# Kernel tuning notes

Hardware: AMD Instinct MI355X
Metric: run time of the kernel (lower is better)

The kernel has to match this reference:

```python
import jax, jax.numpy as jnp
import numpy as np

DMODEL = 1024
NHEAD = 16
HDIM = DMODEL // NHEAD
CTXLEN = 2048
BATCH = 2


def setup_inputs() -> dict:
    key = jax.random.key(0)
    k_x, k_qkv, k_pw, k_pb = jax.random.split(key, 4)
    x = jax.random.normal(k_x, (BATCH, CTXLEN, DMODEL), dtype=jnp.float32)
    # nn.Linear weights: stored as [out, in]; init scale ~ 1/sqrt(in)
    s = 1.0 / np.sqrt(DMODEL)
    w_qkv = jax.random.uniform(k_qkv, (3 * DMODEL, DMODEL), minval=-s, maxval=s, dtype=jnp.float32)
    w_proj = jax.random.uniform(k_pw, (DMODEL, DMODEL), minval=-s, maxval=s, dtype=jnp.float32)
    b_proj = jax.random.uniform(k_pb, (DMODEL,), minval=-s, maxval=s, dtype=jnp.float32)
    return {"x": x, "w_qkv": w_qkv, "w_proj": w_proj, "b_proj": b_proj}


def reference(x, w_qkv, w_proj, b_proj):
    b, t, c = x.shape
    qkv = jnp.einsum('btc,oc->bto', x, w_qkv)  # [b, t, 3c]
    q, k, v = jnp.split(qkv, 3, axis=-1)
    # [b, nhead, t, hdim]
    q = q.reshape(b, t, NHEAD, HDIM).transpose(0, 2, 1, 3)
    k = k.reshape(b, t, NHEAD, HDIM).transpose(0, 2, 1, 3)
    v = v.reshape(b, t, NHEAD, HDIM).transpose(0, 2, 1, 3)
    # NOTE: original code MULTIPLIES by sqrt(hdim) (not the usual divide)
    att = jnp.einsum('bhqd,bhkd->bhqk', q, k) * (HDIM ** 0.5)
    causal = jnp.tril(jnp.ones((t, t), dtype=bool))  # [t, t]
    att = jnp.where(causal[None, None], att, -jnp.inf)
    att = jax.nn.softmax(att, axis=-1)
    y = jnp.einsum('bhqk,bhkd->bhqd', att, v)
    y = y.transpose(0, 2, 1, 3).reshape(b, t, c)
    return jnp.einsum('btc,oc->bto', y, w_proj) + b_proj
```

## Files before the change

### kernel.cpp

```cpp
#include <hip/hip_runtime.h>
#include <hip/hip_bf16.h>

#define DMODEL 1024
#define NHEAD 16
#define HDIM 64
#define CTXLEN 2048
#define BATCH 2
#define M_TOTAL (BATCH * CTXLEN)

typedef unsigned short ushort_t;
typedef __attribute__((ext_vector_type(8))) _Float16 f16x8;
typedef __attribute__((ext_vector_type(8))) unsigned short u16x8;
typedef __attribute__((ext_vector_type(4))) float f32x4;
typedef __attribute__((ext_vector_type(4))) unsigned short u16x4;

#define SCALE_LOG2 11.5415603271f

__device__ __forceinline__ unsigned short f32_f16(float f) {
    return __builtin_bit_cast(unsigned short, (_Float16)f);
}
__device__ __forceinline__ float f16_f32(unsigned short h) {
    return (float)__builtin_bit_cast(_Float16, h);
}
__device__ __forceinline__ float fast_exp2(float x) {
    return __builtin_amdgcn_exp2f(x);
}
__device__ __forceinline__ f32x4 mfma16f(f16x8 a, f16x8 b, f32x4 c) {
    return __builtin_amdgcn_mfma_f32_16x16x32_f16(a, b, c, 0, 0, 0);
}
__device__ __forceinline__ void gload_lds16(const ushort_t* g, ushort_t* l) {
    __builtin_amdgcn_global_load_lds(
        (const __attribute__((address_space(1))) void*)g,
        (__attribute__((address_space(3))) void*)l, 16, 0, 0);
}
__device__ __forceinline__ int unit_off(int qt) {
    if (qt < 8)  return qt;
    if (qt < 16) return 8 + (qt - 8) * 2;
    if (qt < 24) return 24 + (qt - 16) * 3;
    return 48 + (qt - 24) * 4;
}

__global__ __launch_bounds__(256)
void conv3_f32_f16(const float* __restrict__ a, ushort_t* __restrict__ da, int na4,
                   const float* __restrict__ b, ushort_t* __restrict__ db, int nb4,
                   const float* __restrict__ c, ushort_t* __restrict__ dc, int nc4) {
    const int n = na4 + nb4 + nc4;
    for (int i = blockIdx.x * blockDim.x + threadIdx.x; i < n;
         i += gridDim.x * blockDim.x) {
        const float* s; ushort_t* d; int j = i;
        if (j < na4) { s = a; d = da; }
        else if (j - na4 < nb4) { j -= na4; s = b; d = db; }
        else { j -= na4 + nb4; s = c; d = dc; }
        const float4 v = reinterpret_cast<const float4*>(s)[j];
        u16x4 o;
        o[0] = f32_f16(v.x); o[1] = f32_f16(v.y);
        o[2] = f32_f16(v.z); o[3] = f32_f16(v.w);
        reinterpret_cast<u16x4*>(d)[j] = o;
    }
}

template<int BN, bool QKV_EPI>
__global__ __launch_bounds__(256)
void gemm_f16_nt(const ushort_t* __restrict__ A, const ushort_t* __restrict__ B,
                 const float* __restrict__ bias, float* __restrict__ C,
                 ushort_t* __restrict__ qf, ushort_t* __restrict__ kf,
                 ushort_t* __restrict__ vb,
                 int M, int N, int K) {
    constexpr int NF = BN / 32;
    constexpr int BOFF = 8192;
    constexpr int BCHUNK = BN * 8;
    __shared__ ushort_t lds[BOFF + BN * 64];

    int bx, by;
    {
        const int gx  = gridDim.x;
        const int nwg = gx * (int)gridDim.y;
        const int cpx = nwg >> 3;
        int flat = (int)blockIdx.y * gx + (int)blockIdx.x;
        flat = (flat & 7) * cpx + (flat >> 3);
        bx = flat % gx;
        by = flat / gx;
    }

    const int tid  = threadIdx.x;
    const int lane = tid & 63;
    const int wave = tid >> 6;
    const int lc   = lane & 15;
    const int lg   = lane >> 4;
    const int wr   = wave >> 1;
    const int wc   = wave & 1;
    const int row0 = by * 128;
    const int col0 = bx * BN;

    int aoff[4][2], boff[NF][2];
    #pragma unroll
    for (int m = 0; m < 4; ++m) {
        const int ra = wr * 64 + m * 16 + lc;
        #pragma unroll
        for (int kk = 0; kk < 2; ++kk)
            aoff[m][kk] = ra * 64 + (((kk * 4 + lg) ^ (ra & 7)) * 8);
    }
    #pragma unroll
    for (int n = 0; n < NF; ++n) {
        const int rb = wc * (NF * 16) + n * 16 + lc;
        #pragma unroll
        for (int kk = 0; kk < 2; ++kk)
            boff[n][kk] = rb * 64 + (((kk * 4 + lg) ^ (rb & 7)) * 8);
    }

    f32x4 acc[4][NF];
    const f32x4 zero4 = {0.f, 0.f, 0.f, 0.f};
    #pragma unroll
    for (int m = 0; m < 4; ++m)
        #pragma unroll
        for (int n = 0; n < NF; ++n) acc[m][n] = zero4;

    const int NT = K >> 6;

    auto stage = [&](int kt) {
        const int ko = kt * 64;
        #pragma unroll
        for (int i = 0; i < 4; ++i) {
            const int c  = tid + i * 256;
            const int r  = c >> 3;
            const int sg = (c & 7) ^ (r & 7);
            gload_lds16(A + (size_t)(row0 + r) * K + ko + sg * 8, &lds[c * 8]);
        }
        #pragma unroll
        for (int i = 0; i < BCHUNK / 256; ++i) {
            const int c  = tid + i * 256;
            const int r  = c >> 3;
            const int sg = (c & 7) ^ (r & 7);
            gload_lds16(B + (size_t)(col0 + r) * K + ko + sg * 8, &lds[BOFF + c * 8]);
        }
    };

    stage(0);
    for (int kt = 0; kt < NT; ++kt) {
        __syncthreads();
        f16x8 fa[2][4], fb[2][NF];
        #pragma unroll
        for (int kk = 0; kk < 2; ++kk) {
            #pragma unroll
            for (int m = 0; m < 4; ++m)
                fa[kk][m] = *reinterpret_cast<const f16x8*>(&lds[aoff[m][kk]]);
            #pragma unroll
            for (int n = 0; n < NF; ++n)
                fb[kk][n] = *reinterpret_cast<const f16x8*>(&lds[BOFF + boff[n][kk]]);
        }
        __syncthreads();
        if (kt + 1 < NT) stage(kt + 1);
        #pragma unroll
        for (int kk = 0; kk < 2; ++kk)
            #pragma unroll
            for (int m = 0; m < 4; ++m)
                #pragma unroll
                for (int n = 0; n < NF; ++n)
                    acc[m][n] = mfma16f(fa[kk][m], fb[kk][n], acc[m][n]);
    }

    if (!QKV_EPI) {
        #pragma unroll
        for (int m = 0; m < 4; ++m)
            #pragma unroll
            for (int i = 0; i < 4; ++i) {
                const int r = row0 + wr * 64 + m * 16 + lg * 4 + i;
                #pragma unroll
                for (int n = 0; n < NF; ++n) {
                    const int c = col0 + wc * (NF * 16) + n * 16 + lc;
                    C[(size_t)r * N + c] = acc[m][n][i] + bias[c];
                }
            }
    } else {
        #pragma unroll
        for (int m = 0; m < 4; ++m)
            #pragma unroll
            for (int i = 0; i < 4; ++i) {
                const int r = row0 + wr * 64 + m * 16 + lg * 4 + i;
                const int bb = r >> 11;
                const int t  = r & 2047;
                #pragma unroll
                for (int n = 0; n < NF; ++n) {
                    const int cg  = col0 + wc * (NF * 16) + n * 16 + lc;
                    const int sec = cg >> 10;
                    const int ch  = cg & 1023;
                    const int hh  = ch >> 6;
                    const int d   = ch & 63;
                    const size_t off = (((size_t)(bb * NHEAD + hh)) * CTXLEN + t) * HDIM + d;
                    float v = acc[m][n][i];
                    if (sec == 0) v *= SCALE_LOG2;
                    const unsigned short hv = f32_f16(v);
                    if (sec == 0)      qf[off] = hv;
                    else if (sec == 1) kf[off] = hv;
                    else               vb[off] = hv;
                }
            }
    }
}

__global__ __launch_bounds__(256)
void transpose_v(const ushort_t* __restrict__ vb, ushort_t* __restrict__ vt) {
    __shared__ ushort_t T[64][66];
    const int tt = blockIdx.x;
    const int bh = blockIdx.y;
    const int tid = threadIdx.x;
    const int r  = tid >> 2;
    const int c0 = (tid & 3) * 16;

    const ushort_t* src = vb + ((size_t)bh * CTXLEN + tt * 64) * HDIM;
    #pragma unroll
    for (int half = 0; half < 2; ++half) {
        const u16x8 v = *reinterpret_cast<const u16x8*>(&src[(size_t)r * HDIM + c0 + half * 8]);
        #pragma unroll
        for (int j = 0; j < 8; ++j) T[r][c0 + half * 8 + j] = v[j];
    }
    __syncthreads();
    ushort_t* dst = vt + ((size_t)bh * HDIM + r) * CTXLEN + tt * 64 + c0;
    u16x8 o0, o1;
    #pragma unroll
    for (int j = 0; j < 8; ++j) { o0[j] = T[c0 + j][r]; o1[j] = T[c0 + 8 + j][r]; }
    *reinterpret_cast<u16x8*>(&dst[0]) = o0;
    *reinterpret_cast<u16x8*>(&dst[8]) = o1;
}

__global__ __launch_bounds__(256)
void attn_fwd7(const ushort_t* __restrict__ qf, const ushort_t* __restrict__ kf,
               const ushort_t* __restrict__ vt,
               ushort_t* __restrict__ py, float* __restrict__ pml,
               ushort_t* __restrict__ yb) {
    __shared__ ushort_t KH[2][4096];
    __shared__ ushort_t VT[2][4096];
    __shared__ ushort_t Ps[4][16][64];

    const int id    = blockIdx.x;
    const int bh    = id & 31;
    const int u_off = 79 - (id >> 5);
    int qt, u;
    if (u_off < 8)       { qt = u_off;                          u = 0; }
    else if (u_off < 24) { const int t = u_off - 8;  qt = 8  + (t >> 1); u = t & 1; }
    else if (u_off < 48) { const int t = u_off - 24; const int q3 = t / 3; qt = 16 + q3; u = t - q3 * 3; }
    else                 { const int t = u_off - 48; qt = 24 + (t >> 2); u = t & 3; }
    const int total = qt + 1;
    const int nu    = (qt >> 3) + 1;
    const int base  = total / nu, rem = total % nu;
    const int kb0   = u * base + (u < rem ? u : rem);
    const int len   = base + (u < rem ? 1 : 0);
    const int slot  = bh * 80 + u_off;

    const int tid  = threadIdx.x;
    const int wave = tid >> 6;
    const int lane = tid & 63;
    const int lc   = lane & 15;
    const int lg   = lane >> 4;

    const ushort_t* kfb = kf + (size_t)bh * CTXLEN * HDIM;
    const ushort_t* vtb = vt + (size_t)bh * HDIM * CTXLEN;

    const int cA = tid, cB = 256 + tid;
    const int rA = cA >> 3, sgA = (cA & 7) ^ (rA & 7);
    const int rB = cB >> 3, sgB = (cB & 7) ^ (rB & 7);

    auto stage = [&](int kb, int buf) {
        const size_t koff = (size_t)(kb * 64);
        gload_lds16(kfb + (koff + rA) * HDIM + sgA * 8, &KH[buf][cA * 8]);
        gload_lds16(kfb + (koff + rB) * HDIM + sgB * 8, &KH[buf][cB * 8]);
        gload_lds16(vtb + (size_t)rA * CTXLEN + kb * 64 + sgA * 8, &VT[buf][cA * 8]);
        gload_lds16(vtb + (size_t)rB * CTXLEN + kb * 64 + sgB * 8, &VT[buf][cB * 8]);
    };

    const size_t qrow = (size_t)bh * CTXLEN + qt * 64 + wave * 16 + lc;
    f16x8 qfr[2];
    #pragma unroll
    for (int ds = 0; ds < 2; ++ds)
        qfr[ds] = *reinterpret_cast<const f16x8*>(&qf[qrow * HDIM + ds * 32 + lg * 8]);

    const f32x4 zero4 = {0.f, 0.f, 0.f, 0.f};
    f32x4 yacc[4];
    #pragma unroll
    for (int t = 0; t < 4; ++t) yacc[t] = zero4;
    float m_i = -1e30f, l_i = 0.f;

    stage(kb0, 0);
    __syncthreads();

    int cur = 0;
    for (int s = 0; s < len; ++s) {
        const int kb = kb0 + s;
        if (s + 1 < len) stage(kb + 1, cur ^ 1);

        f16x8 kfr[4][2];
        #pragma unroll
        for (int tc = 0; tc < 4; ++tc) {
            const int rk = tc * 16 + lc;
            #pragma unroll
            for (int ds = 0; ds < 2; ++ds) {
                const int a = rk * 64 + (((ds * 4 + lg) ^ (rk & 7)) * 8);
                kfr[tc][ds] = *reinterpret_cast<const f16x8*>(&KH[cur][a]);
            }
        }
        f16x8 vf[4][2];
        #pragma unroll
        for (int t = 0; t < 4; ++t) {
            const int rv = t * 16 + lc;
            #pragma unroll
            for (int ks = 0; ks < 2; ++ks) {
                const int a = rv * 64 + (((ks * 4 + lg) ^ (rv & 7)) * 8);
                vf[t][ks] = *reinterpret_cast<const f16x8*>(&VT[cur][a]);
            }
        }

        f32x4 sacc[4];
        #pragma unroll
        for (int tc = 0; tc < 4; ++tc) sacc[tc] = zero4;
        __builtin_amdgcn_s_setprio(1);
        #pragma unroll
        for (int tc = 0; tc < 4; ++tc)
            #pragma unroll
            for (int ds = 0; ds < 2; ++ds)
                sacc[tc] = mfma16f(kfr[tc][ds], qfr[ds], sacc[tc]);
        __builtin_amdgcn_s_setprio(0);

        float p[4][4];
        #pragma unroll
        for (int tc = 0; tc < 4; ++tc)
            #pragma unroll
            for (int i = 0; i < 4; ++i)
                p[tc][i] = sacc[tc][i];
        if (kb == qt) {
            const int q_loc = wave * 16 + lc;
            #pragma unroll
            for (int tc = 0; tc < 4; ++tc)
                #pragma unroll
                for (int i = 0; i < 4; ++i)
                    if ((tc * 16 + lg * 4 + i) > q_loc) p[tc][i] = -1e30f;
        }
        float mx = p[0][0];
        #pragma unroll
        for (int tc = 0; tc < 4; ++tc)
            #pragma unroll
            for (int i = 0; i < 4; ++i) mx = fmaxf(mx, p[tc][i]);
        mx = fmaxf(mx, __shfl_xor(mx, 16));
        mx = fmaxf(mx, __shfl_xor(mx, 32));

        if (__all(mx <= m_i + 8.0f)) {
            float psum = 0.f;
            #pragma unroll
            for (int tc = 0; tc < 4; ++tc)
                #pragma unroll
                for (int i = 0; i < 4; ++i) {
                    const float e = fast_exp2(p[tc][i] - m_i);
                    p[tc][i] = e;
                    psum += e;
                }
            psum += __shfl_xor(psum, 16);
            psum += __shfl_xor(psum, 32);
            l_i += psum;
        } else {
            const float mnew = fmaxf(m_i, mx);
            const float corr = fast_exp2(m_i - mnew);
            float psum = 0.f;
            #pragma unroll
            for (int tc = 0; tc < 4; ++tc)
                #pragma unroll
                for (int i = 0; i < 4; ++i) {
                    const float e = fast_exp2(p[tc][i] - mnew);
                    p[tc][i] = e;
                    psum += e;
                }
            psum += __shfl_xor(psum, 16);
            psum += __shfl_xor(psum, 32);
            l_i = l_i * corr + psum;
            m_i = mnew;
            #pragma unroll
            for (int t = 0; t < 4; ++t) yacc[t] *= corr;
        }

        #pragma unroll
        for (int tc = 0; tc < 4; ++tc) {
            const int eb = tc * 16 + lg * 4;
            const int se = ((((eb >> 3) ^ (lc & 7)) << 3) | (eb & 7));
            u16x4 pk;
            #pragma unroll
            for (int i = 0; i < 4; ++i) pk[i] = f32_f16(p[tc][i]);
            *reinterpret_cast<u16x4*>(&Ps[wave][lc][se]) = pk;
        }
        f16x8 pa[2];
        #pragma unroll
        for (int ks = 0; ks < 2; ++ks) {
            const int sl = ((ks * 4 + lg) ^ (lc & 7)) << 3;
            pa[ks] = *reinterpret_cast<const f16x8*>(&Ps[wave][lc][sl]);
        }
        __builtin_amdgcn_s_setprio(1);
        #pragma unroll
        for (int t = 0; t < 4; ++t)
            #pragma unroll
            for (int ks = 0; ks < 2; ++ks)
                yacc[t] = mfma16f(vf[t][ks], pa[ks], yacc[t]);
        __builtin_amdgcn_s_setprio(0);

        __syncthreads();
        cur ^= 1;
    }

    const int row = wave * 16 + lc;
    if (nu == 1) {
        const float inv = 1.0f / l_i;
        const int b = bh >> 4, h = bh & 15;
        ushort_t* dst = yb + (size_t)(b * CTXLEN + qt * 64 + row) * DMODEL + h * HDIM;
        #pragma unroll
        for (int t = 0; t < 4; ++t) {
            u16x4 o;
            #pragma unroll
            for (int i = 0; i < 4; ++i) o[i] = f32_f16(yacc[t][i] * inv);
            *reinterpret_cast<u16x4*>(&dst[t * 16 + lg * 4]) = o;
        }
    } else {
        ushort_t* prow = py + ((size_t)slot * 64 + row) * 64;
        #pragma unroll
        for (int t = 0; t < 4; ++t) {
            u16x4 o;
            #pragma unroll
            for (int i = 0; i < 4; ++i) o[i] = f32_f16(yacc[t][i]);
            *reinterpret_cast<u16x4*>(&prow[t * 16 + lg * 4]) = o;
        }
        if (lg == 0) {
            pml[(size_t)slot * 128 + row]      = m_i;
            pml[(size_t)slot * 128 + 64 + row] = l_i;
        }
    }
}

__global__ __launch_bounds__(256)
void merge_attn(const ushort_t* __restrict__ py, const float* __restrict__ pml,
                ushort_t* __restrict__ yb) {
    const int qt  = 8 + blockIdx.x;
    const int bh  = blockIdx.y;
    const int b   = bh >> 4;
    const int h   = bh & 15;
    const int tid = threadIdx.x;
    const int row = tid >> 2;
    const int d0  = (tid & 3) * 16;

    const int nu    = (qt >> 3) + 1;
    const int sbase = bh * 80 + unit_off(qt);

    float mu[4], lu[4];
    float M = -1e30f;
    #pragma unroll
    for (int u = 0; u < 4; ++u) {
        if (u < nu) {
            mu[u] = pml[(size_t)(sbase + u) * 128 + row];
            lu[u] = pml[(size_t)(sbase + u) * 128 + 64 + row];
            M = fmaxf(M, mu[u]);
        } else { mu[u] = -1e30f; lu[u] = 0.f; }
    }
    float w[4], ltot = 0.f;
    #pragma unroll
    for (int u = 0; u < 4; ++u) {
        w[u] = (u < nu) ? fast_exp2(mu[u] - M) : 0.f;
        ltot += w[u] * lu[u];
    }

    float y[16];
    #pragma unroll
    for (int j = 0; j < 16; ++j) y[j] = 0.f;
    #pragma unroll
    for (int u = 0; u < 4; ++u) {
        if (u < nu) {
            const ushort_t* pr = py + ((size_t)(sbase + u) * 64 + row) * 64 + d0;
            const u16x8 a = *reinterpret_cast<const u16x8*>(&pr[0]);
            const u16x8 c = *reinterpret_cast<const u16x8*>(&pr[8]);
            #pragma unroll
            for (int j = 0; j < 8; ++j) {
                y[j]     += w[u] * f16_f32(a[j]);
                y[8 + j] += w[u] * f16_f32(c[j]);
            }
        }
    }
    const float inv = 1.0f / ltot;
    ushort_t* dst = yb + (size_t)(b * CTXLEN + qt * 64 + row) * DMODEL + h * HDIM + d0;
    u16x8 o0, o1;
    #pragma unroll
    for (int j = 0; j < 8; ++j) {
        o0[j] = f32_f16(y[j] * inv);
        o1[j] = f32_f16(y[8 + j] * inv);
    }
    *reinterpret_cast<u16x8*>(&dst[0]) = o0;
    *reinterpret_cast<u16x8*>(&dst[8]) = o1;
}

extern "C" void kernel_launch(void* const* d_in, const int* in_sizes, int n_in,
                              void* d_out, int out_size, void* d_ws, size_t ws_size,
                              hipStream_t stream) {
    const float* x      = (const float*)d_in[0];
    const float* w_qkv  = (const float*)d_in[1];
    const float* w_proj = (const float*)d_in[2];
    const float* b_proj = (const float*)d_in[3];
    float* out = (float*)d_out;

    char* ws = (char*)d_ws;
    ushort_t* wqf = (ushort_t*)(ws);
    ushort_t* wpf = (ushort_t*)(ws + 6291456);
    ushort_t* xf  = (ushort_t*)(ws + 8388608);
    ushort_t* qf  = (ushort_t*)(ws + 16777216);
    ushort_t* kf  = (ushort_t*)(ws + 25165824);
    ushort_t* vb  = (ushort_t*)(ws + 33554432);
    ushort_t* vt  = (ushort_t*)(ws + 41943040);
    ushort_t* py  = (ushort_t*)(ws + 50331648);
    float*    pml = (float*)   (ws + 71303168);
    ushort_t* yb  = xf;

    const dim3 blk(256);

    conv3_f32_f16<<<dim3(2048), blk, 0, stream>>>(
        x, xf, M_TOTAL * DMODEL / 4,
        w_qkv, wqf, 3 * DMODEL * DMODEL / 4,
        w_proj, wpf, DMODEL * DMODEL / 4);

    gemm_f16_nt<128, true><<<dim3(3 * DMODEL / 128, M_TOTAL / 128), blk, 0, stream>>>(
        xf, wqf, nullptr, nullptr, qf, kf, vb, M_TOTAL, 3 * DMODEL, DMODEL);

    transpose_v<<<dim3(CTXLEN / 64, BATCH * NHEAD), blk, 0, stream>>>(vb, vt);

    attn_fwd7<<<dim3(2560), blk, 0, stream>>>(qf, kf, vt, py, pml, yb);
    merge_attn<<<dim3(24, 32), blk, 0, stream>>>(py, pml, yb);

    gemm_f16_nt<64, false><<<dim3(DMODEL / 64, M_TOTAL / 128), blk, 0, stream>>>(
        yb, wpf, b_proj, out, nullptr, nullptr, nullptr, M_TOTAL, DMODEL, DMODEL);
}
```

Before: 108.6 us.

## Fuse V transpose into QKV GEMM epilogue via LDS staging

The QKV GEMM epilogue now stages V-section tiles in shared memory and writes them out directly in transposed [b,h,d,t] layout with vectorized stores. This removes the separate transpose_v kernel launch and its extra global read and write of V. Q and K are still written with per-element scattered stores, now branching on a block-uniform section. The cost is a larger LDS allocation for the QKV GEMM (17408 halves), which may affect occupancy, plus extra barriers in V blocks.

```diff
diff --git a/kernel.cpp b/kernel.cpp
--- a/kernel.cpp
+++ b/kernel.cpp
@@ -64,12 +64,13 @@
 void gemm_f16_nt(const ushort_t* __restrict__ A, const ushort_t* __restrict__ B,
                  const float* __restrict__ bias, float* __restrict__ C,
                  ushort_t* __restrict__ qf, ushort_t* __restrict__ kf,
-                 ushort_t* __restrict__ vb,
+                 ushort_t* __restrict__ vt,
                  int M, int N, int K) {
     constexpr int NF = BN / 32;
     constexpr int BOFF = 8192;
     constexpr int BCHUNK = BN * 8;
-    __shared__ ushort_t lds[BOFF + BN * 64];
+    constexpr int LDSZ = QKV_EPI ? 17408 : (BOFF + BN * 64);
+    __shared__ ushort_t lds[LDSZ];
 
     int bx, by;
     {
@@ -172,55 +173,57 @@
                 }
             }
     } else {
-        #pragma unroll
-        for (int m = 0; m < 4; ++m)
-            #pragma unroll
-            for (int i = 0; i < 4; ++i) {
-                const int r = row0 + wr * 64 + m * 16 + lg * 4 + i;
-                const int bb = r >> 11;
-                const int t  = r & 2047;
+        const int sec_blk = col0 >> 10;
+        if (sec_blk == 2) {
+            __syncthreads();
+            #pragma unroll
+            for (int m = 0; m < 4; ++m)
                 #pragma unroll
                 for (int n = 0; n < NF; ++n) {
-                    const int cg  = col0 + wc * (NF * 16) + n * 16 + lc;
-                    const int sec = cg >> 10;
-                    const int ch  = cg & 1023;
-                    const int hh  = ch >> 6;
-                    const int d   = ch & 63;
-                    const size_t off = (((size_t)(bb * NHEAD + hh)) * CTXLEN + t) * HDIM + d;
-                    float v = acc[m][n][i];
-                    if (sec == 0) v *= SCALE_LOG2;
-                    const unsigned short hv = f32_f16(v);
-                    if (sec == 0)      qf[off] = hv;
-                    else if (sec == 1) kf[off] = hv;
-                    else               vb[off] = hv;
+                    const int lcol = wc * (NF * 16) + n * 16 + lc;
+                    const int lrow = wr * 64 + m * 16 + lg * 4;
+                    u16x4 o;
+                    #pragma unroll
+                    for (int i = 0; i < 4; ++i) o[i] = f32_f16(acc[m][n][i]);
+                    *reinterpret_cast<u16x4*>(&lds[lcol * 136 + lrow]) = o;
                 }
-            }
-    }
-}
-
-__global__ __launch_bounds__(256)
-void transpose_v(const ushort_t* __restrict__ vb, ushort_t* __restrict__ vt) {
-    __shared__ ushort_t T[64][66];
-    const int tt = blockIdx.x;
-    const int bh = blockIdx.y;
-    const int tid = threadIdx.x;
-    const int r  = tid >> 2;
-    const int c0 = (tid & 3) * 16;
-
-    const ushort_t* src = vb + ((size_t)bh * CTXLEN + tt * 64) * HDIM;
-    #pragma unroll
-    for (int half = 0; half < 2; ++half) {
-        const u16x8 v = *reinterpret_cast<const u16x8*>(&src[(size_t)r * HDIM + c0 + half * 8]);
-        #pragma unroll
-        for (int j = 0; j < 8; ++j) T[r][c0 + half * 8 + j] = v[j];
-    }
-    __syncthreads();
-    ushort_t* dst = vt + ((size_t)bh * HDIM + r) * CTXLEN + tt * 64 + c0;
-    u16x8 o0, o1;
-    #pragma unroll
-    for (int j = 0; j < 8; ++j) { o0[j] = T[c0 + j][r]; o1[j] = T[c0 + 8 + j][r]; }
-    *reinterpret_cast<u16x8*>(&dst[0]) = o0;
-    *reinterpret_cast<u16x8*>(&dst[8]) = o1;
+            __syncthreads();
+            const int bb   = row0 >> 11;
+            const int t0   = row0 & 2047;
+            const int lcol = tid >> 1;
+            const int th   = (tid & 1) * 64;
+            const int ch   = (col0 - 2048) + lcol;
+            ushort_t* dst = vt + ((size_t)(bb * NHEAD + (ch >> 6)) * HDIM + (ch & 63)) * CTXLEN
+                            + t0 + th;
+            #pragma unroll
+            for (int j = 0; j < 8; ++j)
+                *reinterpret_cast<u16x8*>(&dst[j * 8]) =
+                    *reinterpret_cast<const u16x8*>(&lds[lcol * 136 + th + j * 8]);
+        } else {
+            #pragma unroll
+            for (int m = 0; m < 4; ++m)
+                #pragma unroll
+                for (int i = 0; i < 4; ++i) {
+                    const int r = row0 + wr * 64 + m * 16 + lg * 4 + i;
+                    const int bb = r >> 11;
+                    const int t  = r & 2047;
+                    #pragma unroll
+                    for (int n = 0; n < NF; ++n) {
+                        const int cg = col0 + wc * (NF * 16) + n * 16 + lc;
+                        const int ch = cg & 1023;
+                        const int hh = ch >> 6;
+                        const int d  = ch & 63;
+                        const size_t off = (((size_t)(bb * NHEAD + hh)) * CTXLEN + t) * HDIM + d;
+                        float v = acc[m][n][i];
+                        if (sec_blk == 0) {
+                            qf[off] = f32_f16(v * SCALE_LOG2);
+                        } else {
+                            kf[off] = f32_f16(v);
+                        }
+                    }
+                }
+        }
+    }
 }
 
 __global__ __launch_bounds__(256)
@@ -504,7 +507,6 @@
     ushort_t* xf  = (ushort_t*)(ws + 8388608);
     ushort_t* qf  = (ushort_t*)(ws + 16777216);
     ushort_t* kf  = (ushort_t*)(ws + 25165824);
-    ushort_t* vb  = (ushort_t*)(ws + 33554432);
     ushort_t* vt  = (ushort_t*)(ws + 41943040);
     ushort_t* py  = (ushort_t*)(ws + 50331648);
     float*    pml = (float*)   (ws + 71303168);
@@ -518,9 +520,7 @@
         w_proj, wpf, DMODEL * DMODEL / 4);
 
     gemm_f16_nt<128, true><<<dim3(3 * DMODEL / 128, M_TOTAL / 128), blk, 0, stream>>>(
-        xf, wqf, nullptr, nullptr, qf, kf, vb, M_TOTAL, 3 * DMODEL, DMODEL);
-
-    transpose_v<<<dim3(CTXLEN / 64, BATCH * NHEAD), blk, 0, stream>>>(vb, vt);
+        xf, wqf, nullptr, nullptr, qf, kf, vt, M_TOTAL, 3 * DMODEL, DMODEL);
 
     attn_fwd7<<<dim3(2560), blk, 0, stream>>>(qf, kf, vt, py, pml, yb);
     merge_attn<<<dim3(24, 32), blk, 0, stream>>>(py, pml, yb);
```

After: 105.3 us (median of 3 runs). 1.03x faster.
